# Performance work log

Measured on AMD Instinct MI355X. Metric: run time of the kernel, lower is better.

## Reference

```python
import jax, jax.numpy as jnp
import numpy as np

N_NODES = 50000
N_EDGES = 800000
F_IN, F_LAT, F_OUT = 64, 64, 64


def _graph_conv(x, W, b, src, dst, deg_out_isqrt, deg_in_isqrt):
    # DGL GraphConv, norm='both': D_out^{-1/2} scaling on src side,
    # linear transform (mult-first since in_feats >= out_feats),
    # scatter-sum to dst, D_in^{-1/2} scaling on dst side, + bias.
    n = x.shape[0]
    h = (x * deg_out_isqrt[:, None]) @ W              # [N, F_out]
    msg = h[src]                                      # [E, F_out] gather
    agg = jax.ops.segment_sum(msg, dst, num_segments=n)  # [N, F_out] scatter
    return agg * deg_in_isqrt[:, None] + b


def setup_inputs() -> dict:
    key = jax.random.key(0)
    ks = jax.random.split(key, 6)
    x = jax.random.normal(ks[0], (N_NODES, F_IN), dtype=jnp.float32)
    W1 = jax.random.normal(ks[1], (F_IN, F_LAT), dtype=jnp.float32) / np.sqrt(F_IN)
    b1 = jnp.zeros((F_LAT,), dtype=jnp.float32)
    W2 = jax.random.normal(ks[2], (F_LAT, F_OUT), dtype=jnp.float32) / np.sqrt(F_LAT)
    b2 = jnp.zeros((F_OUT,), dtype=jnp.float32)
    src = jax.random.randint(ks[3], (N_EDGES,), 0, N_NODES, dtype=jnp.int32)
    dst = jax.random.randint(ks[4], (N_EDGES,), 0, N_NODES, dtype=jnp.int32)
    return {"x": x, "W1": W1, "b1": b1, "W2": W2, "b2": b2, "src": src, "dst": dst}


def reference(x, W1, b1, W2, b2, src, dst):
    n = x.shape[0]
    ones = jnp.ones((src.shape[0],), dtype=x.dtype)
    deg_out = jax.ops.segment_sum(ones, src, num_segments=n)
    deg_in = jax.ops.segment_sum(ones, dst, num_segments=n)
    deg_out_isqrt = jnp.where(deg_out > 0, jax.lax.rsqrt(jnp.maximum(deg_out, 1.0)), 0.0)
    deg_in_isqrt = jnp.where(deg_in > 0, jax.lax.rsqrt(jnp.maximum(deg_in, 1.0)), 0.0)
    h = _graph_conv(x, W1, b1, src, dst, deg_out_isqrt, deg_in_isqrt)
    h = jax.nn.relu(h)
    out = _graph_conv(h, W2, b2, src, dst, deg_out_isqrt, deg_in_isqrt)
    return out
```

## Files before the change

kernel.cpp:

```cpp
#include <hip/hip_runtime.h>

#define NF 64
#define BC 64
#define RANGE 8192

typedef __attribute__((ext_vector_type(8))) short short8;
typedef __attribute__((ext_vector_type(4))) float floatx4;

__device__ __forceinline__ unsigned short f2bf(float f) {
  unsigned int u = __float_as_uint(f);
  return (unsigned short)((u + 0x7fffu + ((u >> 16) & 1u)) >> 16);
}

__global__ __launch_bounds__(256) void hist_kernel(
    const int* __restrict__ src, const int* __restrict__ dst,
    unsigned short* __restrict__ Gout, unsigned short* __restrict__ Gin,
    unsigned char* __restrict__ rank, int n, int nE, int R, int chunk) {
  __shared__ int cnt[RANGE];
  const int rb = blockIdx.x % (R * BC);
  const int kind = blockIdx.x / (R * BC);
  const int r = rb / BC, b = rb % BC;
  const int r0 = r * RANGE;
  for (int i = threadIdx.x; i < RANGE; i += 256) cnt[i] = 0;
  __syncthreads();
  const int lo = b * chunk, hi = min(lo + chunk, nE);
  if (hi <= lo) return;
  const int* keys = kind ? src : dst;
  const int n4 = (hi - lo) >> 2;
  const int4* keys4 = (const int4*)(keys + lo);
  if (kind == 0) {
    for (int i = threadIdx.x; i < n4; i += 256) {
      int4 v = keys4[i];
      int e0 = lo + 4 * i;
      unsigned int k;
      k = (unsigned int)(v.x - r0);
      if (k < (unsigned int)RANGE) rank[e0 + 0] = (unsigned char)atomicAdd(&cnt[k], 1);
      k = (unsigned int)(v.y - r0);
      if (k < (unsigned int)RANGE) rank[e0 + 1] = (unsigned char)atomicAdd(&cnt[k], 1);
      k = (unsigned int)(v.z - r0);
      if (k < (unsigned int)RANGE) rank[e0 + 2] = (unsigned char)atomicAdd(&cnt[k], 1);
      k = (unsigned int)(v.w - r0);
      if (k < (unsigned int)RANGE) rank[e0 + 3] = (unsigned char)atomicAdd(&cnt[k], 1);
    }
    for (int e = lo + 4 * n4 + threadIdx.x; e < hi; e += 256) {
      unsigned int k = (unsigned int)(keys[e] - r0);
      if (k < (unsigned int)RANGE) rank[e] = (unsigned char)atomicAdd(&cnt[k], 1);
    }
    __syncthreads();
    for (int i = threadIdx.x; i < RANGE; i += 256) {
      int nidx = r0 + i;
      if (nidx < n) Gin[(size_t)b * n + nidx] = (unsigned short)cnt[i];
    }
  } else {
    for (int i = threadIdx.x; i < n4; i += 256) {
      int4 v = keys4[i];
      unsigned int k;
      k = (unsigned int)(v.x - r0);
      if (k < (unsigned int)RANGE) atomicAdd(&cnt[k], 1);
      k = (unsigned int)(v.y - r0);
      if (k < (unsigned int)RANGE) atomicAdd(&cnt[k], 1);
      k = (unsigned int)(v.z - r0);
      if (k < (unsigned int)RANGE) atomicAdd(&cnt[k], 1);
      k = (unsigned int)(v.w - r0);
      if (k < (unsigned int)RANGE) atomicAdd(&cnt[k], 1);
    }
    for (int e = lo + 4 * n4 + threadIdx.x; e < hi; e += 256) {
      unsigned int k = (unsigned int)(keys[e] - r0);
      if (k < (unsigned int)RANGE) atomicAdd(&cnt[k], 1);
    }
    __syncthreads();
    for (int i = threadIdx.x; i < RANGE; i += 256) {
      int nidx = r0 + i;
      if (nidx < n) Gout[(size_t)b * n + nidx] = (unsigned short)cnt[i];
    }
  }
}

__global__ __launch_bounds__(256) void colscan_scan1_kernel(
    unsigned short* __restrict__ Gin, const unsigned short* __restrict__ Gout,
    int* __restrict__ deg_in, int* __restrict__ deg_out,
    int* __restrict__ lscan, int* __restrict__ bsum, int n) {
  __shared__ int s[256];
  const int tid = threadIdx.x;
  const int i = blockIdx.x * 256 + tid;
  int di = 0;
  if (i < n) {
    int base = 0;
    #pragma unroll 8
    for (int b = 0; b < BC; ++b) {
      int c = Gin[(size_t)b * n + i];
      Gin[(size_t)b * n + i] = (unsigned short)base;
      base += c;
    }
    di = base;
    int dsum = 0;
    #pragma unroll 8
    for (int b = 0; b < BC; ++b) dsum += Gout[(size_t)b * n + i];
    deg_in[i] = di;
    deg_out[i] = dsum;
  }
  s[tid] = di;
  __syncthreads();
  #pragma unroll
  for (int off = 1; off < 256; off <<= 1) {
    int t2 = (tid >= off) ? s[tid - off] : 0;
    __syncthreads();
    s[tid] += t2;
    __syncthreads();
  }
  if (i < n) lscan[i] = s[tid] - di;
  if (tid == 255) bsum[blockIdx.x] = s[255];
}

__global__ __launch_bounds__(256) void scan3_kernel(
    const int* __restrict__ lscan, const int* __restrict__ bsum,
    const int* __restrict__ deg_out, const int* __restrict__ deg_in,
    const unsigned short* __restrict__ Gin, int* __restrict__ base,
    int* __restrict__ row_start, float* __restrict__ so, float* __restrict__ si,
    int n, int nE) {
  __shared__ int red[256];
  const int tid = threadIdx.x;
  const int b = blockIdx.x;
  red[tid] = (tid < b) ? bsum[tid] : 0;
  __syncthreads();
  #pragma unroll
  for (int s = 128; s > 0; s >>= 1) {
    if (tid < s) red[tid] += red[tid + s];
    __syncthreads();
  }
  const int off = red[0];
  const int i = b * 256 + tid;
  if (b == 0 && tid == 0) row_start[n] = nE;
  if (i < n) {
    int rs = lscan[i] + off;
    row_start[i] = rs;
    int dO = deg_out[i];
    int dI = deg_in[i];
    so[i] = dO > 0 ? rsqrtf((float)dO) : 0.f;
    si[i] = dI > 0 ? rsqrtf((float)dI) : 0.f;
    #pragma unroll 8
    for (int c = 0; c < BC; ++c)
      base[(size_t)c * n + i] = rs + (int)Gin[(size_t)c * n + i];
  }
}

__device__ __forceinline__ void mfma_gemm_core(
    const unsigned short* __restrict__ Ab, const unsigned short* __restrict__ Wt,
    unsigned short* __restrict__ H, int row0, int n, int t) {
  const int w = t >> 6, lane = t & 63;
  const int quad = lane >> 4, l15 = lane & 15;
  const short8 a0 = *(const short8*)&Ab[(w * 16 + l15) * 72 + quad * 8];
  const short8 a1 = *(const short8*)&Ab[(w * 16 + l15) * 72 + 32 + quad * 8];
  #pragma unroll
  for (int cg = 0; cg < 4; ++cg) {
    const short8 b0 = *(const short8*)&Wt[(cg * 16 + l15) * 72 + quad * 8];
    const short8 b1 = *(const short8*)&Wt[(cg * 16 + l15) * 72 + 32 + quad * 8];
    floatx4 acc = {0.f, 0.f, 0.f, 0.f};
    acc = __builtin_amdgcn_mfma_f32_16x16x32_bf16(a0, b0, acc, 0, 0, 0);
    acc = __builtin_amdgcn_mfma_f32_16x16x32_bf16(a1, b1, acc, 0, 0, 0);
    #pragma unroll
    for (int reg = 0; reg < 4; ++reg) {
      int grow = row0 + w * 16 + quad * 4 + reg;
      if (grow < n) H[(size_t)grow * NF + cg * 16 + l15] = f2bf(acc[reg]);
    }
  }
}

__device__ __forceinline__ void stage_wt(
    const float* __restrict__ W, unsigned short* __restrict__ Wt, int t) {
  #pragma unroll
  for (int i = 0; i < 16; ++i) {
    int idx = t + 256 * i;
    int k = idx >> 6, j = idx & 63;
    Wt[j * 72 + k] = f2bf(W[idx]);
  }
}

__global__ __launch_bounds__(256) void place_gemm1_kernel(
    const float* __restrict__ A, const float* __restrict__ so,
    const float* __restrict__ W, unsigned short* __restrict__ H, int n, int ggrid,
    const int* __restrict__ src, const int* __restrict__ dst,
    const unsigned char* __restrict__ rank, const int* __restrict__ base,
    unsigned short* __restrict__ sorted, int nE, int chunk) {
  __shared__ __align__(16) unsigned short Ab[64 * 72];
  __shared__ __align__(16) unsigned short Wt[64 * 72];
  const int t = threadIdx.x;
  if ((int)blockIdx.x >= ggrid) {
    int e = (blockIdx.x - ggrid) * 256 + t;
    if (e < nE) {
      int d = dst[e];
      int b = e / chunk;
      sorted[base[(size_t)b * n + d] + (int)rank[e]] = (unsigned short)src[e];
    }
    return;
  }
  stage_wt(W, Wt, t);
  const int row0 = blockIdx.x * 64;
  #pragma unroll
  for (int i = 0; i < 4; ++i) {
    int idx = t + 256 * i;
    int r = idx >> 4, c4 = idx & 15;
    int gr = row0 + r;
    float4 v = {0.f, 0.f, 0.f, 0.f};
    float s = 0.f;
    if (gr < n) {
      v = *(const float4*)&A[(size_t)gr * NF + c4 * 4];
      s = so[gr];
    }
    ushort4 o;
    o.x = f2bf(v.x * s); o.y = f2bf(v.y * s);
    o.z = f2bf(v.z * s); o.w = f2bf(v.w * s);
    *(ushort4*)&Ab[r * 72 + c4 * 4] = o;
  }
  __syncthreads();
  mfma_gemm_core(Ab, Wt, H, row0, n, t);
}

__global__ __launch_bounds__(256) void gemm2_kernel(
    const unsigned short* __restrict__ Tb, const float* __restrict__ W,
    unsigned short* __restrict__ H, int n) {
  __shared__ __align__(16) unsigned short Ab[64 * 72];
  __shared__ __align__(16) unsigned short Wt[64 * 72];
  const int t = threadIdx.x;
  stage_wt(W, Wt, t);
  const int row0 = blockIdx.x * 64;
  #pragma unroll
  for (int i = 0; i < 4; ++i) {
    int idx = t + 256 * i;
    int r = idx >> 4, c4 = idx & 15;
    int gr = row0 + r;
    ushort4 v = {0, 0, 0, 0};
    if (gr < n) v = *(const ushort4*)&Tb[(size_t)gr * NF + c4 * 4];
    *(ushort4*)&Ab[r * 72 + c4 * 4] = v;
  }
  __syncthreads();
  mfma_gemm_core(Ab, Wt, H, row0, n, t);
}

__device__ __forceinline__ void gather_sum(
    const unsigned short* __restrict__ H, const unsigned short* __restrict__ srcs,
    int beg, int end, int g, int c, float* acc) {
  const float4* Hv = (const float4*)H;
  int e = beg;
  for (; e + 16 <= end; e += 16) {
    int ia = srcs[e + g];
    int ib = srcs[e + 8 + g];
    float4 va = Hv[(size_t)ia * 8 + c];
    float4 vb = Hv[(size_t)ib * 8 + c];
    const unsigned int* pa = (const unsigned int*)&va;
    const unsigned int* pb = (const unsigned int*)&vb;
    #pragma unroll
    for (int k = 0; k < 4; ++k) {
      acc[2 * k]     += __uint_as_float(pa[k] << 16) + __uint_as_float(pb[k] << 16);
      acc[2 * k + 1] += __uint_as_float(pa[k] & 0xffff0000u) + __uint_as_float(pb[k] & 0xffff0000u);
    }
  }
  if (e + 8 <= end) {
    int ia = srcs[e + g];
    float4 va = Hv[(size_t)ia * 8 + c];
    const unsigned int* pa = (const unsigned int*)&va;
    #pragma unroll
    for (int k = 0; k < 4; ++k) {
      acc[2 * k]     += __uint_as_float(pa[k] << 16);
      acc[2 * k + 1] += __uint_as_float(pa[k] & 0xffff0000u);
    }
    e += 8;
  }
  if (e < end) {
    int idx = (e + g < end) ? (e + g) : (end - 1);
    float m = (e + g < end) ? 1.f : 0.f;
    int ia = srcs[idx];
    float4 va = Hv[(size_t)ia * 8 + c];
    const unsigned int* pa = (const unsigned int*)&va;
    #pragma unroll
    for (int k = 0; k < 4; ++k) {
      acc[2 * k]     += m * __uint_as_float(pa[k] << 16);
      acc[2 * k + 1] += m * __uint_as_float(pa[k] & 0xffff0000u);
    }
  }
  #pragma unroll
  for (int d = 8; d <= 32; d <<= 1) {
    #pragma unroll
    for (int k = 0; k < 8; ++k) acc[k] += __shfl_xor(acc[k], d);
  }
}

__global__ __launch_bounds__(256) void agg1_kernel(
    const unsigned short* __restrict__ H1, const int* __restrict__ row_start,
    const unsigned short* __restrict__ srcs, const float* __restrict__ si,
    const float* __restrict__ so, const float* __restrict__ b1,
    unsigned short* __restrict__ T, int n) {
  int node = blockIdx.x * 4 + (threadIdx.x >> 6);
  if (node >= n) return;
  const int lane = threadIdx.x & 63;
  const int g = lane >> 3;
  const int c = lane & 7;
  float acc[8] = {0, 0, 0, 0, 0, 0, 0, 0};
  gather_sum(H1, srcs, row_start[node], row_start[node + 1], g, c, acc);
  if (g == 0) {
    const float sin = si[node];
    const float son = so[node];
    ushort4 o0, o1;
    float v;
    v = fmaxf(fmaf(acc[0], sin, b1[c * 8 + 0]), 0.f) * son; o0.x = f2bf(v);
    v = fmaxf(fmaf(acc[1], sin, b1[c * 8 + 1]), 0.f) * son; o0.y = f2bf(v);
    v = fmaxf(fmaf(acc[2], sin, b1[c * 8 + 2]), 0.f) * son; o0.z = f2bf(v);
    v = fmaxf(fmaf(acc[3], sin, b1[c * 8 + 3]), 0.f) * son; o0.w = f2bf(v);
    v = fmaxf(fmaf(acc[4], sin, b1[c * 8 + 4]), 0.f) * son; o1.x = f2bf(v);
    v = fmaxf(fmaf(acc[5], sin, b1[c * 8 + 5]), 0.f) * son; o1.y = f2bf(v);
    v = fmaxf(fmaf(acc[6], sin, b1[c * 8 + 6]), 0.f) * son; o1.z = f2bf(v);
    v = fmaxf(fmaf(acc[7], sin, b1[c * 8 + 7]), 0.f) * son; o1.w = f2bf(v);
    *(ushort4*)&T[(size_t)node * NF + c * 8]     = o0;
    *(ushort4*)&T[(size_t)node * NF + c * 8 + 4] = o1;
  }
}

__global__ __launch_bounds__(256) void agg2_kernel(
    const unsigned short* __restrict__ H2, const int* __restrict__ row_start,
    const unsigned short* __restrict__ srcs, const float* __restrict__ si,
    const float* __restrict__ b2, float* __restrict__ out, int n) {
  int node = blockIdx.x * 4 + (threadIdx.x >> 6);
  if (node >= n) return;
  const int lane = threadIdx.x & 63;
  const int g = lane >> 3;
  const int c = lane & 7;
  float acc[8] = {0, 0, 0, 0, 0, 0, 0, 0};
  gather_sum(H2, srcs, row_start[node], row_start[node + 1], g, c, acc);
  if (g == 0) {
    const float sin = si[node];
    const float4 b4a = *(const float4*)&b2[c * 8];
    const float4 b4b = *(const float4*)&b2[c * 8 + 4];
    float4 r0, r1;
    r0.x = fmaf(acc[0], sin, b4a.x);
    r0.y = fmaf(acc[1], sin, b4a.y);
    r0.z = fmaf(acc[2], sin, b4a.z);
    r0.w = fmaf(acc[3], sin, b4a.w);
    r1.x = fmaf(acc[4], sin, b4b.x);
    r1.y = fmaf(acc[5], sin, b4b.y);
    r1.z = fmaf(acc[6], sin, b4b.z);
    r1.w = fmaf(acc[7], sin, b4b.w);
    *(float4*)&out[(size_t)node * NF + c * 8]     = r0;
    *(float4*)&out[(size_t)node * NF + c * 8 + 4] = r1;
  }
}

extern "C" void kernel_launch(void* const* d_in, const int* in_sizes, int n_in,
                              void* d_out, int out_size, void* d_ws, size_t ws_size,
                              hipStream_t stream) {
  const float* x  = (const float*)d_in[0];
  const float* W1 = (const float*)d_in[1];
  const float* b1 = (const float*)d_in[2];
  const float* W2 = (const float*)d_in[3];
  const float* b2 = (const float*)d_in[4];
  const int* src  = (const int*)d_in[5];
  const int* dst  = (const int*)d_in[6];
  float* out = (float*)d_out;

  const int N = in_sizes[0] / NF;
  const int E = in_sizes[5];
  const int NB = (N + 255) / 256;
  const int R  = (N + RANGE - 1) / RANGE;
  const int CH = (((E + BC - 1) / BC) + 3) & ~3;

  char* ws = (char*)d_ws;
  size_t p = 0;
  auto alloc = [&](size_t bytes) -> void* {
    void* r = ws + p;
    p = (p + bytes + 255) & ~(size_t)255;
    return r;
  };
  int*   deg_out_i  = (int*)  alloc((size_t)N * 4);
  int*   deg_in_i   = (int*)  alloc((size_t)N * 4);
  float* so         = (float*)alloc((size_t)N * 4);
  float* si         = (float*)alloc((size_t)N * 4);
  int*   row_start  = (int*)  alloc((size_t)(N + 1) * 4);
  int*   bsum       = (int*)  alloc((size_t)NB * 4);
  int*   lscan      = (int*)  alloc((size_t)N * 4);
  unsigned short* sorted_u16 = (unsigned short*)alloc((size_t)E * 2);
  unsigned char*  rank  = (unsigned char*)alloc((size_t)E);
  unsigned short* h1    = (unsigned short*)alloc((size_t)N * NF * 2);
  unsigned short* G_in  = (unsigned short*)alloc((size_t)BC * N * 2);
  unsigned short* tb    = (unsigned short*)alloc((size_t)N * NF * 2);
  unsigned short* G_out = (unsigned short*)alloc((size_t)BC * N * 2);
  int* base = (int*)tb;
  unsigned short* h2 = h1;

  hist_kernel<<<2 * R * BC, 256, 0, stream>>>(src, dst, G_out, G_in, rank,
                                              N, E, R, CH);

  colscan_scan1_kernel<<<NB, 256, 0, stream>>>(G_in, G_out, deg_in_i, deg_out_i,
                                               lscan, bsum, N);

  scan3_kernel<<<NB, 256, 0, stream>>>(lscan, bsum, deg_out_i, deg_in_i,
                                       G_in, base, row_start, so, si, N, E);

  const int ggrid = (N + 63) / 64;
  const int pgrid = (E + 255) / 256;
  const int agrid = (N + 3) / 4;

  place_gemm1_kernel<<<ggrid + pgrid, 256, 0, stream>>>(
      x, so, W1, h1, N, ggrid, src, dst, rank, base, sorted_u16, E, CH);

  agg1_kernel<<<agrid, 256, 0, stream>>>(h1, row_start, sorted_u16, si, so, b1, tb, N);

  gemm2_kernel<<<ggrid, 256, 0, stream>>>(tb, W2, h2, N);

  agg2_kernel<<<agrid, 256, 0, stream>>>(h2, row_start, sorted_u16, si, b2, out, N);
}
```

Measured before the change: 185.1 us.

## Pack histogram counters into bytes and split gather aggregation into source-half passes

The histogram now packs four 8-bit counters per shared-memory word, which doubles the node range per block and halves the G_in/G_out traffic by storing bytes. Each aggregation is split into two passes that each gather only sources from one half of the node range, so the working set of H fits better in cache. The first pass writes fp32 partial sums to a new buffer P, and the second pass adds them and finishes. This costs extra kernel launches, a second full read of the edge lists, a round trip of P through memory, and wasted lanes on masked edges. The 8-bit counters overflow if any node takes more than 255 edges within one chunk.

After: 216.6 us. 17.0% more time.

```diff
diff --git a/kernel.cpp b/kernel.cpp
--- a/kernel.cpp
+++ b/kernel.cpp
@@ -2,7 +2,8 @@
 
 #define NF 64
 #define BC 64
-#define RANGE 8192
+#define RANGE 16384
+#define RWORDS (RANGE / 4)
 
 typedef __attribute__((ext_vector_type(8))) short short8;
 typedef __attribute__((ext_vector_type(4))) float floatx4;
@@ -14,70 +15,71 @@
 
 __global__ __launch_bounds__(256) void hist_kernel(
     const int* __restrict__ src, const int* __restrict__ dst,
-    unsigned short* __restrict__ Gout, unsigned short* __restrict__ Gin,
+    unsigned char* __restrict__ Gout, unsigned char* __restrict__ Gin,
     unsigned char* __restrict__ rank, int n, int nE, int R, int chunk) {
-  __shared__ int cnt[RANGE];
+  __shared__ int cnt[RWORDS];
   const int rb = blockIdx.x % (R * BC);
   const int kind = blockIdx.x / (R * BC);
   const int r = rb / BC, b = rb % BC;
   const int r0 = r * RANGE;
-  for (int i = threadIdx.x; i < RANGE; i += 256) cnt[i] = 0;
+  for (int i = threadIdx.x; i < RWORDS; i += 256) cnt[i] = 0;
   __syncthreads();
   const int lo = b * chunk, hi = min(lo + chunk, nE);
-  if (hi <= lo) return;
   const int* keys = kind ? src : dst;
-  const int n4 = (hi - lo) >> 2;
+  const int n4 = (hi > lo) ? ((hi - lo) >> 2) : 0;
   const int4* keys4 = (const int4*)(keys + lo);
   if (kind == 0) {
     for (int i = threadIdx.x; i < n4; i += 256) {
       int4 v = keys4[i];
       int e0 = lo + 4 * i;
-      unsigned int k;
+      unsigned int k, old, sh;
       k = (unsigned int)(v.x - r0);
-      if (k < (unsigned int)RANGE) rank[e0 + 0] = (unsigned char)atomicAdd(&cnt[k], 1);
+      if (k < (unsigned int)RANGE) { sh = (k & 3) * 8; old = atomicAdd(&cnt[k >> 2], 1u << sh); rank[e0 + 0] = (unsigned char)(old >> sh); }
       k = (unsigned int)(v.y - r0);
-      if (k < (unsigned int)RANGE) rank[e0 + 1] = (unsigned char)atomicAdd(&cnt[k], 1);
+      if (k < (unsigned int)RANGE) { sh = (k & 3) * 8; old = atomicAdd(&cnt[k >> 2], 1u << sh); rank[e0 + 1] = (unsigned char)(old >> sh); }
       k = (unsigned int)(v.z - r0);
-      if (k < (unsigned int)RANGE) rank[e0 + 2] = (unsigned char)atomicAdd(&cnt[k], 1);
+      if (k < (unsigned int)RANGE) { sh = (k & 3) * 8; old = atomicAdd(&cnt[k >> 2], 1u << sh); rank[e0 + 2] = (unsigned char)(old >> sh); }
       k = (unsigned int)(v.w - r0);
-      if (k < (unsigned int)RANGE) rank[e0 + 3] = (unsigned char)atomicAdd(&cnt[k], 1);
+      if (k < (unsigned int)RANGE) { sh = (k & 3) * 8; old = atomicAdd(&cnt[k >> 2], 1u << sh); rank[e0 + 3] = (unsigned char)(old >> sh); }
     }
     for (int e = lo + 4 * n4 + threadIdx.x; e < hi; e += 256) {
       unsigned int k = (unsigned int)(keys[e] - r0);
-      if (k < (unsigned int)RANGE) rank[e] = (unsigned char)atomicAdd(&cnt[k], 1);
+      if (k < (unsigned int)RANGE) {
+        unsigned int sh = (k & 3) * 8;
+        unsigned int old = atomicAdd(&cnt[k >> 2], 1u << sh);
+        rank[e] = (unsigned char)(old >> sh);
+      }
     }
     __syncthreads();
-    for (int i = threadIdx.x; i < RANGE; i += 256) {
-      int nidx = r0 + i;
-      if (nidx < n) Gin[(size_t)b * n + nidx] = (unsigned short)cnt[i];
-    }
+    unsigned int* Gw = (unsigned int*)(Gin + (size_t)b * n + r0);
+    for (int i = threadIdx.x; i < RWORDS; i += 256)
+      if (r0 + 4 * i < n) Gw[i] = (unsigned int)cnt[i];
   } else {
     for (int i = threadIdx.x; i < n4; i += 256) {
       int4 v = keys4[i];
       unsigned int k;
       k = (unsigned int)(v.x - r0);
-      if (k < (unsigned int)RANGE) atomicAdd(&cnt[k], 1);
+      if (k < (unsigned int)RANGE) atomicAdd(&cnt[k >> 2], 1u << ((k & 3) * 8));
       k = (unsigned int)(v.y - r0);
-      if (k < (unsigned int)RANGE) atomicAdd(&cnt[k], 1);
+      if (k < (unsigned int)RANGE) atomicAdd(&cnt[k >> 2], 1u << ((k & 3) * 8));
       k = (unsigned int)(v.z - r0);
-      if (k < (unsigned int)RANGE) atomicAdd(&cnt[k], 1);
+      if (k < (unsigned int)RANGE) atomicAdd(&cnt[k >> 2], 1u << ((k & 3) * 8));
       k = (unsigned int)(v.w - r0);
-      if (k < (unsigned int)RANGE) atomicAdd(&cnt[k], 1);
+      if (k < (unsigned int)RANGE) atomicAdd(&cnt[k >> 2], 1u << ((k & 3) * 8));
     }
     for (int e = lo + 4 * n4 + threadIdx.x; e < hi; e += 256) {
       unsigned int k = (unsigned int)(keys[e] - r0);
-      if (k < (unsigned int)RANGE) atomicAdd(&cnt[k], 1);
+      if (k < (unsigned int)RANGE) atomicAdd(&cnt[k >> 2], 1u << ((k & 3) * 8));
     }
     __syncthreads();
-    for (int i = threadIdx.x; i < RANGE; i += 256) {
-      int nidx = r0 + i;
-      if (nidx < n) Gout[(size_t)b * n + nidx] = (unsigned short)cnt[i];
-    }
+    unsigned int* Gw = (unsigned int*)(Gout + (size_t)b * n + r0);
+    for (int i = threadIdx.x; i < RWORDS; i += 256)
+      if (r0 + 4 * i < n) Gw[i] = (unsigned int)cnt[i];
   }
 }
 
 __global__ __launch_bounds__(256) void colscan_scan1_kernel(
-    unsigned short* __restrict__ Gin, const unsigned short* __restrict__ Gout,
+    unsigned char* __restrict__ Gin, const unsigned char* __restrict__ Gout,
     int* __restrict__ deg_in, int* __restrict__ deg_out,
     int* __restrict__ lscan, int* __restrict__ bsum, int n) {
   __shared__ int s[256];
@@ -89,7 +91,7 @@
     #pragma unroll 8
     for (int b = 0; b < BC; ++b) {
       int c = Gin[(size_t)b * n + i];
-      Gin[(size_t)b * n + i] = (unsigned short)base;
+      Gin[(size_t)b * n + i] = (unsigned char)base;
       base += c;
     }
     di = base;
@@ -115,7 +117,7 @@
 __global__ __launch_bounds__(256) void scan3_kernel(
     const int* __restrict__ lscan, const int* __restrict__ bsum,
     const int* __restrict__ deg_out, const int* __restrict__ deg_in,
-    const unsigned short* __restrict__ Gin, int* __restrict__ base,
+    const unsigned char* __restrict__ Gin, int* __restrict__ base,
     int* __restrict__ row_start, float* __restrict__ so, float* __restrict__ si,
     int n, int nE) {
   __shared__ int red[256];
@@ -237,45 +239,55 @@
   mfma_gemm_core(Ab, Wt, H, row0, n, t);
 }
 
-__device__ __forceinline__ void gather_sum(
+template <int PASS>
+__device__ __forceinline__ void gather_sliced(
     const unsigned short* __restrict__ H, const unsigned short* __restrict__ srcs,
-    int beg, int end, int g, int c, float* acc) {
+    int beg, int end, int g, int c, int half, float* acc) {
   const float4* Hv = (const float4*)H;
   int e = beg;
   for (; e + 16 <= end; e += 16) {
     int ia = srcs[e + g];
     int ib = srcs[e + 8 + g];
-    float4 va = Hv[(size_t)ia * 8 + c];
-    float4 vb = Hv[(size_t)ib * 8 + c];
+    float ma = ((ia < half) == (PASS == 0)) ? 1.f : 0.f;
+    float mb = ((ib < half) == (PASS == 0)) ? 1.f : 0.f;
+    int iae = (ma != 0.f) ? ia : 0;
+    int ibe = (mb != 0.f) ? ib : 0;
+    float4 va = Hv[(size_t)iae * 8 + c];
+    float4 vb = Hv[(size_t)ibe * 8 + c];
     const unsigned int* pa = (const unsigned int*)&va;
     const unsigned int* pb = (const unsigned int*)&vb;
     #pragma unroll
     for (int k = 0; k < 4; ++k) {
-      acc[2 * k]     += __uint_as_float(pa[k] << 16) + __uint_as_float(pb[k] << 16);
-      acc[2 * k + 1] += __uint_as_float(pa[k] & 0xffff0000u) + __uint_as_float(pb[k] & 0xffff0000u);
+      acc[2 * k]     = fmaf(ma, __uint_as_float(pa[k] << 16), acc[2 * k]);
+      acc[2 * k]     = fmaf(mb, __uint_as_float(pb[k] << 16), acc[2 * k]);
+      acc[2 * k + 1] = fmaf(ma, __uint_as_float(pa[k] & 0xffff0000u), acc[2 * k + 1]);
+      acc[2 * k + 1] = fmaf(mb, __uint_as_float(pb[k] & 0xffff0000u), acc[2 * k + 1]);
     }
   }
   if (e + 8 <= end) {
     int ia = srcs[e + g];
-    float4 va = Hv[(size_t)ia * 8 + c];
+    float ma = ((ia < half) == (PASS == 0)) ? 1.f : 0.f;
+    int iae = (ma != 0.f) ? ia : 0;
+    float4 va = Hv[(size_t)iae * 8 + c];
     const unsigned int* pa = (const unsigned int*)&va;
     #pragma unroll
     for (int k = 0; k < 4; ++k) {
-      acc[2 * k]     += __uint_as_float(pa[k] << 16);
-      acc[2 * k + 1] += __uint_as_float(pa[k] & 0xffff0000u);
+      acc[2 * k]     = fmaf(ma, __uint_as_float(pa[k] << 16), acc[2 * k]);
+      acc[2 * k + 1] = fmaf(ma, __uint_as_float(pa[k] & 0xffff0000u), acc[2 * k + 1]);
     }
     e += 8;
   }
   if (e < end) {
     int idx = (e + g < end) ? (e + g) : (end - 1);
-    float m = (e + g < end) ? 1.f : 0.f;
     int ia = srcs[idx];
-    float4 va = Hv[(size_t)ia * 8 + c];
+    float m = ((e + g < end) && ((ia < half) == (PASS == 0))) ? 1.f : 0.f;
+    int iae = (m != 0.f) ? ia : 0;
+    float4 va = Hv[(size_t)iae * 8 + c];
     const unsigned int* pa = (const unsigned int*)&va;
     #pragma unroll
     for (int k = 0; k < 4; ++k) {
-      acc[2 * k]     += m * __uint_as_float(pa[k] << 16);
-      acc[2 * k + 1] += m * __uint_as_float(pa[k] & 0xffff0000u);
+      acc[2 * k]     = fmaf(m, __uint_as_float(pa[k] << 16), acc[2 * k]);
+      acc[2 * k + 1] = fmaf(m, __uint_as_float(pa[k] & 0xffff0000u), acc[2 * k + 1]);
     }
   }
   #pragma unroll
@@ -285,60 +297,76 @@
   }
 }
 
+template <int PASS>
 __global__ __launch_bounds__(256) void agg1_kernel(
     const unsigned short* __restrict__ H1, const int* __restrict__ row_start,
     const unsigned short* __restrict__ srcs, const float* __restrict__ si,
     const float* __restrict__ so, const float* __restrict__ b1,
-    unsigned short* __restrict__ T, int n) {
+    float* __restrict__ P, unsigned short* __restrict__ T, int n, int half) {
   int node = blockIdx.x * 4 + (threadIdx.x >> 6);
   if (node >= n) return;
   const int lane = threadIdx.x & 63;
   const int g = lane >> 3;
   const int c = lane & 7;
   float acc[8] = {0, 0, 0, 0, 0, 0, 0, 0};
-  gather_sum(H1, srcs, row_start[node], row_start[node + 1], g, c, acc);
-  if (g == 0) {
+  gather_sliced<PASS>(H1, srcs, row_start[node], row_start[node + 1], g, c, half, acc);
+  if (g != 0) return;
+  if (PASS == 0) {
+    *(float4*)&P[(size_t)node * NF + c * 8]     = make_float4(acc[0], acc[1], acc[2], acc[3]);
+    *(float4*)&P[(size_t)node * NF + c * 8 + 4] = make_float4(acc[4], acc[5], acc[6], acc[7]);
+  } else {
+    const float4 p0 = *(const float4*)&P[(size_t)node * NF + c * 8];
+    const float4 p1 = *(const float4*)&P[(size_t)node * NF + c * 8 + 4];
+    const float pp[8] = {p0.x, p0.y, p0.z, p0.w, p1.x, p1.y, p1.z, p1.w};
     const float sin = si[node];
     const float son = so[node];
     ushort4 o0, o1;
     float v;
-    v = fmaxf(fmaf(acc[0], sin, b1[c * 8 + 0]), 0.f) * son; o0.x = f2bf(v);
-    v = fmaxf(fmaf(acc[1], sin, b1[c * 8 + 1]), 0.f) * son; o0.y = f2bf(v);
-    v = fmaxf(fmaf(acc[2], sin, b1[c * 8 + 2]), 0.f) * son; o0.z = f2bf(v);
-    v = fmaxf(fmaf(acc[3], sin, b1[c * 8 + 3]), 0.f) * son; o0.w = f2bf(v);
-    v = fmaxf(fmaf(acc[4], sin, b1[c * 8 + 4]), 0.f) * son; o1.x = f2bf(v);
-    v = fmaxf(fmaf(acc[5], sin, b1[c * 8 + 5]), 0.f) * son; o1.y = f2bf(v);
-    v = fmaxf(fmaf(acc[6], sin, b1[c * 8 + 6]), 0.f) * son; o1.z = f2bf(v);
-    v = fmaxf(fmaf(acc[7], sin, b1[c * 8 + 7]), 0.f) * son; o1.w = f2bf(v);
+    v = fmaxf(fmaf(acc[0] + pp[0], sin, b1[c * 8 + 0]), 0.f) * son; o0.x = f2bf(v);
+    v = fmaxf(fmaf(acc[1] + pp[1], sin, b1[c * 8 + 1]), 0.f) * son; o0.y = f2bf(v);
+    v = fmaxf(fmaf(acc[2] + pp[2], sin, b1[c * 8 + 2]), 0.f) * son; o0.z = f2bf(v);
+    v = fmaxf(fmaf(acc[3] + pp[3], sin, b1[c * 8 + 3]), 0.f) * son; o0.w = f2bf(v);
+    v = fmaxf(fmaf(acc[4] + pp[4], sin, b1[c * 8 + 4]), 0.f) * son; o1.x = f2bf(v);
+    v = fmaxf(fmaf(acc[5] + pp[5], sin, b1[c * 8 + 5]), 0.f) * son; o1.y = f2bf(v);
+    v = fmaxf(fmaf(acc[6] + pp[6], sin, b1[c * 8 + 6]), 0.f) * son; o1.z = f2bf(v);
+    v = fmaxf(fmaf(acc[7] + pp[7], sin, b1[c * 8 + 7]), 0.f) * son; o1.w = f2bf(v);
     *(ushort4*)&T[(size_t)node * NF + c * 8]     = o0;
     *(ushort4*)&T[(size_t)node * NF + c * 8 + 4] = o1;
   }
 }
 
+template <int PASS>
 __global__ __launch_bounds__(256) void agg2_kernel(
     const unsigned short* __restrict__ H2, const int* __restrict__ row_start,
     const unsigned short* __restrict__ srcs, const float* __restrict__ si,
-    const float* __restrict__ b2, float* __restrict__ out, int n) {
+    const float* __restrict__ b2, float* __restrict__ P,
+    float* __restrict__ out, int n, int half) {
   int node = blockIdx.x * 4 + (threadIdx.x >> 6);
   if (node >= n) return;
   const int lane = threadIdx.x & 63;
   const int g = lane >> 3;
   const int c = lane & 7;
   float acc[8] = {0, 0, 0, 0, 0, 0, 0, 0};
-  gather_sum(H2, srcs, row_start[node], row_start[node + 1], g, c, acc);
-  if (g == 0) {
+  gather_sliced<PASS>(H2, srcs, row_start[node], row_start[node + 1], g, c, half, acc);
+  if (g != 0) return;
+  if (PASS == 0) {
+    *(float4*)&P[(size_t)node * NF + c * 8]     = make_float4(acc[0], acc[1], acc[2], acc[3]);
+    *(float4*)&P[(size_t)node * NF + c * 8 + 4] = make_float4(acc[4], acc[5], acc[6], acc[7]);
+  } else {
+    const float4 p0 = *(const float4*)&P[(size_t)node * NF + c * 8];
+    const float4 p1 = *(const float4*)&P[(size_t)node * NF + c * 8 + 4];
     const float sin = si[node];
     const float4 b4a = *(const float4*)&b2[c * 8];
     const float4 b4b = *(const float4*)&b2[c * 8 + 4];
     float4 r0, r1;
-    r0.x = fmaf(acc[0], sin, b4a.x);
-    r0.y = fmaf(acc[1], sin, b4a.y);
-    r0.z = fmaf(acc[2], sin, b4a.z);
-    r0.w = fmaf(acc[3], sin, b4a.w);
-    r1.x = fmaf(acc[4], sin, b4b.x);
-    r1.y = fmaf(acc[5], sin, b4b.y);
-    r1.z = fmaf(acc[6], sin, b4b.z);
-    r1.w = fmaf(acc[7], sin, b4b.w);
+    r0.x = fmaf(acc[0] + p0.x, sin, b4a.x);
+    r0.y = fmaf(acc[1] + p0.y, sin, b4a.y);
+    r0.z = fmaf(acc[2] + p0.z, sin, b4a.z);
+    r0.w = fmaf(acc[3] + p0.w, sin, b4a.w);
+    r1.x = fmaf(acc[4] + p1.x, sin, b4b.x);
+    r1.y = fmaf(acc[5] + p1.y, sin, b4b.y);
+    r1.z = fmaf(acc[6] + p1.z, sin, b4b.z);
+    r1.w = fmaf(acc[7] + p1.w, sin, b4b.w);
     *(float4*)&out[(size_t)node * NF + c * 8]     = r0;
     *(float4*)&out[(size_t)node * NF + c * 8 + 4] = r1;
   }
@@ -361,6 +389,7 @@
   const int NB = (N + 255) / 256;
   const int R  = (N + RANGE - 1) / RANGE;
   const int CH = (((E + BC - 1) / BC) + 3) & ~3;
+  const int HALF = N / 2;
 
   char* ws = (char*)d_ws;
   size_t p = 0;
@@ -379,9 +408,10 @@
   unsigned short* sorted_u16 = (unsigned short*)alloc((size_t)E * 2);
   unsigned char*  rank  = (unsigned char*)alloc((size_t)E);
   unsigned short* h1    = (unsigned short*)alloc((size_t)N * NF * 2);
-  unsigned short* G_in  = (unsigned short*)alloc((size_t)BC * N * 2);
+  unsigned char*  G_in  = (unsigned char*)alloc((size_t)BC * N);
   unsigned short* tb    = (unsigned short*)alloc((size_t)N * NF * 2);
-  unsigned short* G_out = (unsigned short*)alloc((size_t)BC * N * 2);
+  unsigned char*  G_out = (unsigned char*)alloc((size_t)BC * N);
+  float*          P     = (float*)alloc((size_t)N * NF * 4);
   int* base = (int*)tb;
   unsigned short* h2 = h1;
 
@@ -401,9 +431,11 @@
   place_gemm1_kernel<<<ggrid + pgrid, 256, 0, stream>>>(
       x, so, W1, h1, N, ggrid, src, dst, rank, base, sorted_u16, E, CH);
 
-  agg1_kernel<<<agrid, 256, 0, stream>>>(h1, row_start, sorted_u16, si, so, b1, tb, N);
+  agg1_kernel<0><<<agrid, 256, 0, stream>>>(h1, row_start, sorted_u16, si, so, b1, P, tb, N, HALF);
+  agg1_kernel<1><<<agrid, 256, 0, stream>>>(h1, row_start, sorted_u16, si, so, b1, P, tb, N, HALF);
 
   gemm2_kernel<<<ggrid, 256, 0, stream>>>(tb, W2, h2, N);
 
-  agg2_kernel<<<agrid, 256, 0, stream>>>(h2, row_start, sorted_u16, si, b2, out, N);
-}
+  agg2_kernel<0><<<agrid, 256, 0, stream>>>(h2, row_start, sorted_u16, si, b2, P, out, N, HALF);
+  agg2_kernel<1><<<agrid, 256, 0, stream>>>(h2, row_start, sorted_u16, si, b2, P, out, N, HALF);
+}
```

## Pack per-chunk node histograms into byte counters and split base fill into own kernel

Applied to the files above, without the earlier changes.

Histogram counters are packed four 8-bit counts per shared-memory word, doubling the node range per block (fewer histogram blocks) and halving the size of the per-chunk count matrices written to global memory. Degree rsqrt normalisation moves into the column-scan kernel, removing the separate degree arrays. The per-chunk base offsets are now computed in a new fully parallel kernel instead of a serial 64-iteration loop per thread, at the cost of an extra launch and a dedicated base buffer. Byte counters overflow if any node receives more than 255 edges within one chunk, which assumes a low-degree random graph.

After: 183.2 us. No clear change (-1.0%).

```diff
diff --git a/kernel.cpp b/kernel.cpp
--- a/kernel.cpp
+++ b/kernel.cpp
@@ -2,7 +2,8 @@
 
 #define NF 64
 #define BC 64
-#define RANGE 8192
+#define RANGE 16384
+#define RWORDS (RANGE / 4)
 
 typedef __attribute__((ext_vector_type(8))) short short8;
 typedef __attribute__((ext_vector_type(4))) float floatx4;
@@ -14,71 +15,72 @@
 
 __global__ __launch_bounds__(256) void hist_kernel(
     const int* __restrict__ src, const int* __restrict__ dst,
-    unsigned short* __restrict__ Gout, unsigned short* __restrict__ Gin,
+    unsigned char* __restrict__ Gout, unsigned char* __restrict__ Gin,
     unsigned char* __restrict__ rank, int n, int nE, int R, int chunk) {
-  __shared__ int cnt[RANGE];
+  __shared__ int cnt[RWORDS];
   const int rb = blockIdx.x % (R * BC);
   const int kind = blockIdx.x / (R * BC);
   const int r = rb / BC, b = rb % BC;
   const int r0 = r * RANGE;
-  for (int i = threadIdx.x; i < RANGE; i += 256) cnt[i] = 0;
+  for (int i = threadIdx.x; i < RWORDS; i += 256) cnt[i] = 0;
   __syncthreads();
   const int lo = b * chunk, hi = min(lo + chunk, nE);
-  if (hi <= lo) return;
   const int* keys = kind ? src : dst;
-  const int n4 = (hi - lo) >> 2;
+  const int n4 = (hi > lo) ? ((hi - lo) >> 2) : 0;
   const int4* keys4 = (const int4*)(keys + lo);
   if (kind == 0) {
     for (int i = threadIdx.x; i < n4; i += 256) {
       int4 v = keys4[i];
       int e0 = lo + 4 * i;
-      unsigned int k;
+      unsigned int k, old, sh;
       k = (unsigned int)(v.x - r0);
-      if (k < (unsigned int)RANGE) rank[e0 + 0] = (unsigned char)atomicAdd(&cnt[k], 1);
+      if (k < (unsigned int)RANGE) { sh = (k & 3) * 8; old = atomicAdd(&cnt[k >> 2], 1u << sh); rank[e0 + 0] = (unsigned char)(old >> sh); }
       k = (unsigned int)(v.y - r0);
-      if (k < (unsigned int)RANGE) rank[e0 + 1] = (unsigned char)atomicAdd(&cnt[k], 1);
+      if (k < (unsigned int)RANGE) { sh = (k & 3) * 8; old = atomicAdd(&cnt[k >> 2], 1u << sh); rank[e0 + 1] = (unsigned char)(old >> sh); }
       k = (unsigned int)(v.z - r0);
-      if (k < (unsigned int)RANGE) rank[e0 + 2] = (unsigned char)atomicAdd(&cnt[k], 1);
+      if (k < (unsigned int)RANGE) { sh = (k & 3) * 8; old = atomicAdd(&cnt[k >> 2], 1u << sh); rank[e0 + 2] = (unsigned char)(old >> sh); }
       k = (unsigned int)(v.w - r0);
-      if (k < (unsigned int)RANGE) rank[e0 + 3] = (unsigned char)atomicAdd(&cnt[k], 1);
+      if (k < (unsigned int)RANGE) { sh = (k & 3) * 8; old = atomicAdd(&cnt[k >> 2], 1u << sh); rank[e0 + 3] = (unsigned char)(old >> sh); }
     }
     for (int e = lo + 4 * n4 + threadIdx.x; e < hi; e += 256) {
       unsigned int k = (unsigned int)(keys[e] - r0);
-      if (k < (unsigned int)RANGE) rank[e] = (unsigned char)atomicAdd(&cnt[k], 1);
+      if (k < (unsigned int)RANGE) {
+        unsigned int sh = (k & 3) * 8;
+        unsigned int old = atomicAdd(&cnt[k >> 2], 1u << sh);
+        rank[e] = (unsigned char)(old >> sh);
+      }
     }
     __syncthreads();
-    for (int i = threadIdx.x; i < RANGE; i += 256) {
-      int nidx = r0 + i;
-      if (nidx < n) Gin[(size_t)b * n + nidx] = (unsigned short)cnt[i];
-    }
+    unsigned int* Gw = (unsigned int*)(Gin + (size_t)b * n + r0);
+    for (int i = threadIdx.x; i < RWORDS; i += 256)
+      if (r0 + 4 * i < n) Gw[i] = (unsigned int)cnt[i];
   } else {
     for (int i = threadIdx.x; i < n4; i += 256) {
       int4 v = keys4[i];
       unsigned int k;
       k = (unsigned int)(v.x - r0);
-      if (k < (unsigned int)RANGE) atomicAdd(&cnt[k], 1);
+      if (k < (unsigned int)RANGE) atomicAdd(&cnt[k >> 2], 1u << ((k & 3) * 8));
       k = (unsigned int)(v.y - r0);
-      if (k < (unsigned int)RANGE) atomicAdd(&cnt[k], 1);
+      if (k < (unsigned int)RANGE) atomicAdd(&cnt[k >> 2], 1u << ((k & 3) * 8));
       k = (unsigned int)(v.z - r0);
-      if (k < (unsigned int)RANGE) atomicAdd(&cnt[k], 1);
+      if (k < (unsigned int)RANGE) atomicAdd(&cnt[k >> 2], 1u << ((k & 3) * 8));
       k = (unsigned int)(v.w - r0);
-      if (k < (unsigned int)RANGE) atomicAdd(&cnt[k], 1);
+      if (k < (unsigned int)RANGE) atomicAdd(&cnt[k >> 2], 1u << ((k & 3) * 8));
     }
     for (int e = lo + 4 * n4 + threadIdx.x; e < hi; e += 256) {
       unsigned int k = (unsigned int)(keys[e] - r0);
-      if (k < (unsigned int)RANGE) atomicAdd(&cnt[k], 1);
+      if (k < (unsigned int)RANGE) atomicAdd(&cnt[k >> 2], 1u << ((k & 3) * 8));
     }
     __syncthreads();
-    for (int i = threadIdx.x; i < RANGE; i += 256) {
-      int nidx = r0 + i;
-      if (nidx < n) Gout[(size_t)b * n + nidx] = (unsigned short)cnt[i];
-    }
+    unsigned int* Gw = (unsigned int*)(Gout + (size_t)b * n + r0);
+    for (int i = threadIdx.x; i < RWORDS; i += 256)
+      if (r0 + 4 * i < n) Gw[i] = (unsigned int)cnt[i];
   }
 }
 
 __global__ __launch_bounds__(256) void colscan_scan1_kernel(
-    unsigned short* __restrict__ Gin, const unsigned short* __restrict__ Gout,
-    int* __restrict__ deg_in, int* __restrict__ deg_out,
+    unsigned char* __restrict__ Gin, const unsigned char* __restrict__ Gout,
+    float* __restrict__ so, float* __restrict__ si,
     int* __restrict__ lscan, int* __restrict__ bsum, int n) {
   __shared__ int s[256];
   const int tid = threadIdx.x;
@@ -89,15 +91,15 @@
     #pragma unroll 8
     for (int b = 0; b < BC; ++b) {
       int c = Gin[(size_t)b * n + i];
-      Gin[(size_t)b * n + i] = (unsigned short)base;
+      Gin[(size_t)b * n + i] = (unsigned char)base;
       base += c;
     }
     di = base;
     int dsum = 0;
     #pragma unroll 8
     for (int b = 0; b < BC; ++b) dsum += Gout[(size_t)b * n + i];
-    deg_in[i] = di;
-    deg_out[i] = dsum;
+    si[i] = di > 0 ? rsqrtf((float)di) : 0.f;
+    so[i] = dsum > 0 ? rsqrtf((float)dsum) : 0.f;
   }
   s[tid] = di;
   __syncthreads();
@@ -114,10 +116,7 @@
 
 __global__ __launch_bounds__(256) void scan3_kernel(
     const int* __restrict__ lscan, const int* __restrict__ bsum,
-    const int* __restrict__ deg_out, const int* __restrict__ deg_in,
-    const unsigned short* __restrict__ Gin, int* __restrict__ base,
-    int* __restrict__ row_start, float* __restrict__ so, float* __restrict__ si,
-    int n, int nE) {
+    int* __restrict__ row_start, int n, int nE) {
   __shared__ int red[256];
   const int tid = threadIdx.x;
   const int b = blockIdx.x;
@@ -131,17 +130,15 @@
   const int off = red[0];
   const int i = b * 256 + tid;
   if (b == 0 && tid == 0) row_start[n] = nE;
-  if (i < n) {
-    int rs = lscan[i] + off;
-    row_start[i] = rs;
-    int dO = deg_out[i];
-    int dI = deg_in[i];
-    so[i] = dO > 0 ? rsqrtf((float)dO) : 0.f;
-    si[i] = dI > 0 ? rsqrtf((float)dI) : 0.f;
-    #pragma unroll 8
-    for (int c = 0; c < BC; ++c)
-      base[(size_t)c * n + i] = rs + (int)Gin[(size_t)c * n + i];
-  }
+  if (i < n) row_start[i] = lscan[i] + off;
+}
+
+__global__ __launch_bounds__(256) void basefill_kernel(
+    const int* __restrict__ row_start, const unsigned char* __restrict__ Gin,
+    int* __restrict__ base, int n, int nb) {
+  const int c = blockIdx.x / nb;
+  const int i = (blockIdx.x % nb) * 256 + threadIdx.x;
+  if (i < n) base[(size_t)c * n + i] = row_start[i] + (int)Gin[(size_t)c * n + i];
 }
 
 __device__ __forceinline__ void mfma_gemm_core(
@@ -361,6 +358,7 @@
   const int NB = (N + 255) / 256;
   const int R  = (N + RANGE - 1) / RANGE;
   const int CH = (((E + BC - 1) / BC) + 3) & ~3;
+  (void)ws_size;
 
   char* ws = (char*)d_ws;
   size_t p = 0;
@@ -369,8 +367,6 @@
     p = (p + bytes + 255) & ~(size_t)255;
     return r;
   };
-  int*   deg_out_i  = (int*)  alloc((size_t)N * 4);
-  int*   deg_in_i   = (int*)  alloc((size_t)N * 4);
   float* so         = (float*)alloc((size_t)N * 4);
   float* si         = (float*)alloc((size_t)N * 4);
   int*   row_start  = (int*)  alloc((size_t)(N + 1) * 4);
@@ -379,20 +375,21 @@
   unsigned short* sorted_u16 = (unsigned short*)alloc((size_t)E * 2);
   unsigned char*  rank  = (unsigned char*)alloc((size_t)E);
   unsigned short* h1    = (unsigned short*)alloc((size_t)N * NF * 2);
-  unsigned short* G_in  = (unsigned short*)alloc((size_t)BC * N * 2);
+  unsigned char*  G_in  = (unsigned char*)alloc((size_t)BC * N);
+  unsigned char*  G_out = (unsigned char*)alloc((size_t)BC * N);
   unsigned short* tb    = (unsigned short*)alloc((size_t)N * NF * 2);
-  unsigned short* G_out = (unsigned short*)alloc((size_t)BC * N * 2);
-  int* base = (int*)tb;
+  int*            base  = (int*)alloc((size_t)BC * N * 4);
   unsigned short* h2 = h1;
 
   hist_kernel<<<2 * R * BC, 256, 0, stream>>>(src, dst, G_out, G_in, rank,
                                               N, E, R, CH);
 
-  colscan_scan1_kernel<<<NB, 256, 0, stream>>>(G_in, G_out, deg_in_i, deg_out_i,
+  colscan_scan1_kernel<<<NB, 256, 0, stream>>>(G_in, G_out, so, si,
                                                lscan, bsum, N);
 
-  scan3_kernel<<<NB, 256, 0, stream>>>(lscan, bsum, deg_out_i, deg_in_i,
-                                       G_in, base, row_start, so, si, N, E);
+  scan3_kernel<<<NB, 256, 0, stream>>>(lscan, bsum, row_start, N, E);
+
+  basefill_kernel<<<BC * NB, 256, 0, stream>>>(row_start, G_in, base, N, NB);
 
   const int ggrid = (N + 63) / 64;
   const int pgrid = (E + 255) / 256;
```
